# Optimization experiments

Measured on AMD Instinct MI355X. Metric: run time of the kernel, lower is better.

The kernel has to match this reference:

```python
import jax, jax.numpy as jnp
import numpy as np

B, T, C = 4, 2048, 1024
H, D = 16, 64  # n_heads, head_dim; C == H*D

def setup_inputs() -> dict:
    key = jax.random.key(0)
    ks = jax.random.split(key, 6)
    s_in = 1.0 / np.sqrt(C)
    x = jax.random.normal(ks[0], (B, T, C), dtype=jnp.float32)
    # causal mask: True above the diagonal -> masked to -inf
    mask = jnp.triu(jnp.ones((T, T), dtype=bool), k=1)
    Wqkv = jax.random.uniform(ks[1], (C, 3 * C), jnp.float32, -s_in, s_in)
    bqkv = jax.random.uniform(ks[2], (3 * C,), jnp.float32, -s_in, s_in)
    Wout = jax.random.uniform(ks[3], (C, C), jnp.float32, -s_in, s_in)
    bout = jax.random.uniform(ks[4], (C,), jnp.float32, -s_in, s_in)
    return {"x": x, "mask": mask, "Wqkv": Wqkv, "bqkv": bqkv, "Wout": Wout, "bout": bout}

def reference(x, mask, Wqkv, bqkv, Wout, bout):
    b, t, c = x.shape
    qkv = (x @ Wqkv + bqkv).reshape(b, t, 3, H, D)
    qkv = jnp.transpose(qkv, (2, 0, 3, 1, 4))  # [3, B, H, T, D]
    q, k, v = qkv[0], qkv[1], qkv[2]
    scores = jnp.einsum("bhqd,bhkd->bhqk", q, k) / jnp.sqrt(jnp.float32(D))
    scores = jnp.where(mask[:t, :t][None, None, :, :], -jnp.inf, scores)
    attn = jax.nn.softmax(scores, axis=-1)
    out = jnp.einsum("bhqk,bhkd->bhqd", attn, v)
    out = jnp.transpose(out, (0, 2, 1, 3)).reshape(b, t, c)
    return out @ Wout + bout
```

## Files before the change

### kernel.cpp

```cpp
#include <hip/hip_runtime.h>

typedef unsigned short u16;
typedef __attribute__((ext_vector_type(8))) short bf16x8;
typedef __attribute__((ext_vector_type(4))) short bf16x4;
typedef __attribute__((ext_vector_type(4))) float f32x4;

#define MFMA16(a, b, c) __builtin_amdgcn_mfma_f32_16x16x32_bf16(a, b, c, 0, 0, 0)

__device__ __forceinline__ u16 f2bf(float x) {
    unsigned u = __float_as_uint(x);
    return (u16)((u + 0x7fffu + ((u >> 16) & 1u)) >> 16);
}
__device__ __forceinline__ u16 f2bf_fast(float x) {
    return (u16)((__float_as_uint(x) + 0x8000u) >> 16);
}

__global__ __launch_bounds__(256) void castk(const float* __restrict__ src, u16* __restrict__ dst) {
    const int i = (blockIdx.x * 256 + threadIdx.x) * 8;
    float4 a = *(const float4*)(src + i);
    float4 b = *(const float4*)(src + i + 4);
    bf16x8 v;
    v[0] = (short)f2bf(a.x); v[1] = (short)f2bf(a.y);
    v[2] = (short)f2bf(a.z); v[3] = (short)f2bf(a.w);
    v[4] = (short)f2bf(b.x); v[5] = (short)f2bf(b.y);
    v[6] = (short)f2bf(b.z); v[7] = (short)f2bf(b.w);
    *(bf16x8*)(dst + i) = v;
}

__global__ __launch_bounds__(256) void tkern(const float* __restrict__ src, u16* __restrict__ dst,
                                             int R, int C) {
    const int tC = C >> 6;
    const int tr = (blockIdx.x / tC) << 6;
    const int tc = (blockIdx.x % tC) << 6;
    __shared__ u16 ls[64 * 68];
    const int tid = threadIdx.x;
#pragma unroll
    for (int rep = 0; rep < 2; ++rep) {
        const int f = tid * 8 + rep * 2048;
        const int r = f >> 6, c = f & 63;
        float4 a = *(const float4*)(src + (size_t)(tr + r) * C + tc + c);
        float4 b = *(const float4*)(src + (size_t)(tr + r) * C + tc + c + 4);
        bf16x4 lo, hi;
        lo[0] = (short)f2bf(a.x); lo[1] = (short)f2bf(a.y);
        lo[2] = (short)f2bf(a.z); lo[3] = (short)f2bf(a.w);
        hi[0] = (short)f2bf(b.x); hi[1] = (short)f2bf(b.y);
        hi[2] = (short)f2bf(b.z); hi[3] = (short)f2bf(b.w);
        *(bf16x4*)&ls[r * 68 + c] = lo;
        *(bf16x4*)&ls[r * 68 + c + 4] = hi;
    }
    __syncthreads();
#pragma unroll
    for (int rep = 0; rep < 2; ++rep) {
        const int f = tid * 8 + rep * 2048;
        const int rn = f >> 6, ck = f & 63;
        bf16x8 v;
#pragma unroll
        for (int j = 0; j < 8; ++j) v[j] = (short)ls[(ck + j) * 68 + rn];
        *(bf16x8*)(dst + (size_t)(tc + rn) * R + tr + ck) = v;
    }
}

template <int MODE>
__global__ __launch_bounds__(256) void gemm_k(const u16* __restrict__ A, const u16* __restrict__ Bt,
                                              const float* __restrict__ bias,
                                              u16* __restrict__ Qo, u16* __restrict__ Ko,
                                              u16* __restrict__ Vo, float* __restrict__ Of) {
    constexpr int Kd = 1024;
    const int tid = threadIdx.x;
    const int lane = tid & 63, wave = tid >> 6;
    const int wm = wave >> 1, wn = wave & 1;
    const int lr = lane & 15, lg = lane >> 4;
    const int mt = blockIdx.x & 63;
    const int nt = blockIdx.x >> 6;
    const int mbase = mt << 7, nbase = nt << 7;
    __shared__ u16 As[128 * 32];
    __shared__ u16 Bs[128 * 32];
    f32x4 acc[4][4];
#pragma unroll
    for (int i = 0; i < 4; ++i)
#pragma unroll
        for (int j = 0; j < 4; ++j) acc[i][j] = {0.f, 0.f, 0.f, 0.f};

    for (int kb = 0; kb < Kd; kb += 32) {
        __syncthreads();
#pragma unroll
        for (int rep = 0; rep < 2; ++rep) {
            const int f = tid * 8 + rep * 2048;
            const int r = f >> 5, c = f & 31;
            __builtin_amdgcn_global_load_lds(
                (const __attribute__((address_space(1))) void*)(A + (size_t)(mbase + r) * Kd + kb + c),
                (__attribute__((address_space(3))) void*)(As + f), 16, 0, 0);
            __builtin_amdgcn_global_load_lds(
                (const __attribute__((address_space(1))) void*)(Bt + (size_t)(nbase + r) * Kd + kb + c),
                (__attribute__((address_space(3))) void*)(Bs + f), 16, 0, 0);
        }
        __syncthreads();
        bf16x8 af[4], bfr[4];
#pragma unroll
        for (int i = 0; i < 4; ++i)
            af[i] = *(const bf16x8*)&As[(wm * 64 + i * 16 + lr) * 32 + lg * 8];
#pragma unroll
        for (int j = 0; j < 4; ++j)
            bfr[j] = *(const bf16x8*)&Bs[(wn * 64 + j * 16 + lr) * 32 + lg * 8];
#pragma unroll
        for (int i = 0; i < 4; ++i)
#pragma unroll
            for (int j = 0; j < 4; ++j) acc[i][j] = MFMA16(af[i], bfr[j], acc[i][j]);
    }

    const float QSCALE = 0.1803368801111137f;
#pragma unroll
    for (int j = 0; j < 4; ++j) {
        const int n = nbase + wn * 64 + j * 16 + lr;
        const float bj = bias[n];
        if (MODE == 0) {
            const int three = n >> 10;
            const int h = (n >> 6) & 15;
            const int d = n & 63;
#pragma unroll
            for (int i = 0; i < 4; ++i) {
#pragma unroll
                for (int r = 0; r < 4; ++r) {
                    const int m = mbase + wm * 64 + i * 16 + lg * 4 + r;
                    const int b = m >> 11, t = m & 2047;
                    const int bh = (b << 4) + h;
                    const float val = acc[i][j][r] + bj;
                    if (three == 0)
                        Qo[(((size_t)bh << 11) + t) * 64 + d] = f2bf(val * QSCALE);
                    else if (three == 1)
                        Ko[(((size_t)bh << 11) + t) * 64 + d] = f2bf(val);
                    else
                        Vo[(((size_t)bh << 6) + d) * 2048 + t] = f2bf(val);
                }
            }
        } else {
#pragma unroll
            for (int i = 0; i < 4; ++i) {
#pragma unroll
                for (int r = 0; r < 4; ++r) {
                    const int m = mbase + wm * 64 + i * 16 + lg * 4 + r;
                    Of[((size_t)m << 10) + n] = acc[i][j][r] + bj;
                }
            }
        }
    }
}

__global__ __launch_bounds__(128, 2) void flash_attn(const u16* __restrict__ Q, const u16* __restrict__ Kg,
                                                     const u16* __restrict__ Vt, u16* __restrict__ Aout) {
    const int tid = threadIdx.x;
    const int lane = tid & 63, wave = tid >> 6;
    const int lr = lane & 15, lg = lane >> 4;
    const int bx = blockIdx.x;
    const int bh = blockIdx.y;
    const int b = bh >> 4, h = bh & 15;
    const size_t base = (size_t)bh << 17;

    const int qb_hi = 16 + bx;
    const int qb_lo = 15 - bx;

    __shared__ u16 Ps[2][16 * 72];

    int qbase[4];
    qbase[0] = qb_hi * 64 + wave * 32;
    qbase[1] = qbase[0] + 16;
    qbase[2] = qb_lo * 64 + wave * 32;
    qbase[3] = qbase[2] + 16;

    bf16x8 qf[4][2];
#pragma unroll
    for (int st = 0; st < 4; ++st) {
        const u16* p = Q + base + (size_t)(qbase[st] + lr) * 64;
        qf[st][0] = *(const bf16x8*)(p + lg * 8);
        qf[st][1] = *(const bf16x8*)(p + 32 + lg * 8);
    }

    f32x4 o[4][4];
#pragma unroll
    for (int st = 0; st < 4; ++st)
#pragma unroll
        for (int dt = 0; dt < 4; ++dt) o[st][dt] = {0.f, 0.f, 0.f, 0.f};
    float m_[4] = {-INFINITY, -INFINITY, -INFINITY, -INFINITY};
    float l_[4] = {0.f, 0.f, 0.f, 0.f};

    const u16* Kbase = Kg + base + (size_t)lr * 64 + lg * 8;
    const u16* Vbase = Vt + base + (size_t)lr * 2048 + lg * 8;

    for (int kt = 0; kt <= qb_hi; ++kt) {
        bf16x8 kf[4][2], vf[4][2];
        const u16* kp = Kbase + (size_t)kt * 4096;
#pragma unroll
        for (int rt = 0; rt < 4; ++rt) {
            kf[rt][0] = *(const bf16x8*)(kp + rt * 1024);
            kf[rt][1] = *(const bf16x8*)(kp + rt * 1024 + 32);
        }
        const u16* vp = Vbase + kt * 64;
#pragma unroll
        for (int dt = 0; dt < 4; ++dt) {
            vf[dt][0] = *(const bf16x8*)(vp + dt * 32768);
            vf[dt][1] = *(const bf16x8*)(vp + dt * 32768 + 32);
        }

        auto process = [&](int st, bool diag) {
            f32x4 s[4];
#pragma unroll
            for (int rt = 0; rt < 4; ++rt) {
                f32x4 z = {0.f, 0.f, 0.f, 0.f};
                z = MFMA16(kf[rt][0], qf[st][0], z);
                z = MFMA16(kf[rt][1], qf[st][1], z);
                s[rt] = z;
            }
            if (diag) {
                const int q_glob = qbase[st] + lr;
#pragma unroll
                for (int rt = 0; rt < 4; ++rt)
#pragma unroll
                    for (int r = 0; r < 4; ++r) {
                        const int kv = kt * 64 + rt * 16 + lg * 4 + r;
                        if (kv > q_glob) s[rt][r] = -INFINITY;
                    }
            }
            float rmax = -INFINITY;
#pragma unroll
            for (int rt = 0; rt < 4; ++rt)
#pragma unroll
                for (int r = 0; r < 4; ++r) rmax = fmaxf(rmax, s[rt][r]);
            rmax = fmaxf(rmax, __shfl_xor(rmax, 16));
            rmax = fmaxf(rmax, __shfl_xor(rmax, 32));
            const float m_new = fmaxf(m_[st], rmax);
            const float alpha = exp2f(m_[st] - m_new);
            float rsum = 0.f;
#pragma unroll
            for (int rt = 0; rt < 4; ++rt)
#pragma unroll
                for (int r = 0; r < 4; ++r) {
                    const float p = exp2f(s[rt][r] - m_new);
                    s[rt][r] = p;
                    rsum += p;
                }
            rsum += __shfl_xor(rsum, 16);
            rsum += __shfl_xor(rsum, 32);
            l_[st] = l_[st] * alpha + rsum;
            m_[st] = m_new;

#pragma unroll
            for (int rt = 0; rt < 4; ++rt) {
                bf16x4 pk;
#pragma unroll
                for (int r = 0; r < 4; ++r) pk[r] = (short)f2bf_fast(s[rt][r]);
                *(bf16x4*)&Ps[wave][lr * 72 + rt * 16 + lg * 4] = pk;
            }
            float aq[4];
#pragma unroll
            for (int r = 0; r < 4; ++r) aq[r] = __shfl(alpha, (lane & 48) + lg * 4 + r);
#pragma unroll
            for (int dt = 0; dt < 4; ++dt)
#pragma unroll
                for (int r = 0; r < 4; ++r) o[st][dt][r] *= aq[r];

            const bf16x8 pf0 = *(const bf16x8*)&Ps[wave][lr * 72 + lg * 8];
            const bf16x8 pf1 = *(const bf16x8*)&Ps[wave][lr * 72 + 32 + lg * 8];
#pragma unroll
            for (int dt = 0; dt < 4; ++dt) {
                o[st][dt] = MFMA16(pf0, vf[dt][0], o[st][dt]);
                o[st][dt] = MFMA16(pf1, vf[dt][1], o[st][dt]);
            }
        };

        process(0, kt == qb_hi);
        process(1, kt == qb_hi);
        if (kt <= qb_lo) {
            process(2, kt == qb_lo);
            process(3, kt == qb_lo);
        }
    }

#pragma unroll
    for (int st = 0; st < 4; ++st) {
        const float linv = 1.f / l_[st];
        float lq[4];
#pragma unroll
        for (int r = 0; r < 4; ++r) lq[r] = __shfl(linv, (lane & 48) + lg * 4 + r);
#pragma unroll
        for (int dt = 0; dt < 4; ++dt)
#pragma unroll
            for (int r = 0; r < 4; ++r) {
                const int t = qbase[st] + lg * 4 + r;
                Aout[(((size_t)(b << 11) + t) << 10) + h * 64 + dt * 16 + lr] =
                    f2bf(o[st][dt][r] * lq[r]);
            }
    }
}

extern "C" void kernel_launch(void* const* d_in, const int* in_sizes, int n_in,
                              void* d_out, int out_size, void* d_ws, size_t ws_size,
                              hipStream_t stream) {
    (void)in_sizes; (void)n_in; (void)out_size; (void)ws_size;
    const float* x    = (const float*)d_in[0];
    const float* Wqkv = (const float*)d_in[2];
    const float* bqkv = (const float*)d_in[3];
    const float* Wout = (const float*)d_in[4];
    const float* bout = (const float*)d_in[5];
    float* out = (float*)d_out;

    char* ws = (char*)d_ws;
    u16* WqkvT = (u16*)(ws);
    u16* WoutT = (u16*)(ws + 6291456);
    u16* xb    = (u16*)(ws + 8388608);
    u16* Qb    = (u16*)(ws + 25165824);
    u16* Kb    = (u16*)(ws + 41943040);
    u16* Vtb   = (u16*)(ws + 58720256);
    u16* Ab    = (u16*)(ws + 75497472);

    castk<<<dim3(4096), 256, 0, stream>>>(x, xb);
    tkern<<<dim3(16 * 48), 256, 0, stream>>>(Wqkv, WqkvT, 1024, 3072);
    tkern<<<dim3(16 * 16), 256, 0, stream>>>(Wout, WoutT, 1024, 1024);
    gemm_k<0><<<dim3(64 * 24), 256, 0, stream>>>(xb, WqkvT, bqkv, Qb, Kb, Vtb, nullptr);
    flash_attn<<<dim3(16, 64), 128, 0, stream>>>(Qb, Kb, Vtb, Ab);
    gemm_k<1><<<dim3(64 * 8), 256, 0, stream>>>(Ab, WoutT, bout, nullptr, nullptr, nullptr, out);
}
```

Before: 336.9 us.

## Double-buffer K loads and transpose PV MFMA to drop alpha shuffles

Prefetches the next K tile into a second register buffer while the current tile is processed. It swaps the MFMA operand order for P·V so each lane holds output rows matching its own softmax statistics. That removes the alpha and 1/l shuffles and allows vectorized 4-wide bf16 stores of the output. The rescale of O is also skipped when no row's max changed, at the cost of higher register pressure from the double buffer.

```diff
diff --git a/kernel.cpp b/kernel.cpp
--- a/kernel.cpp
+++ b/kernel.cpp
@@ -186,14 +186,21 @@
     const u16* Kbase = Kg + base + (size_t)lr * 64 + lg * 8;
     const u16* Vbase = Vt + base + (size_t)lr * 2048 + lg * 8;
 
-    for (int kt = 0; kt <= qb_hi; ++kt) {
-        bf16x8 kf[4][2], vf[4][2];
+    auto loadK = [&](int kt, bf16x8 (&kf)[4][2]) {
         const u16* kp = Kbase + (size_t)kt * 4096;
 #pragma unroll
         for (int rt = 0; rt < 4; ++rt) {
             kf[rt][0] = *(const bf16x8*)(kp + rt * 1024);
             kf[rt][1] = *(const bf16x8*)(kp + rt * 1024 + 32);
         }
+    };
+
+    bf16x8 kfA[4][2], kfB[4][2];
+    loadK(0, kfA);
+
+    auto iter = [&](int kt, bf16x8 (&kf)[4][2], bf16x8 (&kfN)[4][2]) {
+        loadK(kt < qb_hi ? kt + 1 : qb_hi, kfN);
+        bf16x8 vf[4][2];
         const u16* vp = Vbase + kt * 64;
 #pragma unroll
         for (int dt = 0; dt < 4; ++dt) {
@@ -250,20 +257,18 @@
                 for (int r = 0; r < 4; ++r) pk[r] = (short)f2bf_fast(s[rt][r]);
                 *(bf16x4*)&Ps[wave][lr * 72 + rt * 16 + lg * 4] = pk;
             }
-            float aq[4];
-#pragma unroll
-            for (int r = 0; r < 4; ++r) aq[r] = __shfl(alpha, (lane & 48) + lg * 4 + r);
-#pragma unroll
-            for (int dt = 0; dt < 4; ++dt)
-#pragma unroll
-                for (int r = 0; r < 4; ++r) o[st][dt][r] *= aq[r];
-
+            if (__any(alpha != 1.0f)) {
+#pragma unroll
+                for (int dt = 0; dt < 4; ++dt)
+#pragma unroll
+                    for (int r = 0; r < 4; ++r) o[st][dt][r] *= alpha;
+            }
             const bf16x8 pf0 = *(const bf16x8*)&Ps[wave][lr * 72 + lg * 8];
             const bf16x8 pf1 = *(const bf16x8*)&Ps[wave][lr * 72 + 32 + lg * 8];
 #pragma unroll
             for (int dt = 0; dt < 4; ++dt) {
-                o[st][dt] = MFMA16(pf0, vf[dt][0], o[st][dt]);
-                o[st][dt] = MFMA16(pf1, vf[dt][1], o[st][dt]);
+                o[st][dt] = MFMA16(vf[dt][0], pf0, o[st][dt]);
+                o[st][dt] = MFMA16(vf[dt][1], pf1, o[st][dt]);
             }
         };
 
@@ -273,22 +278,27 @@
             process(2, kt == qb_lo);
             process(3, kt == qb_lo);
         }
+    };
+
+    for (int kt = 0; kt <= qb_hi;) {
+        iter(kt, kfA, kfB);
+        ++kt;
+        if (kt > qb_hi) break;
+        iter(kt, kfB, kfA);
+        ++kt;
     }
 
 #pragma unroll
     for (int st = 0; st < 4; ++st) {
         const float linv = 1.f / l_[st];
-        float lq[4];
-#pragma unroll
-        for (int r = 0; r < 4; ++r) lq[r] = __shfl(linv, (lane & 48) + lg * 4 + r);
-#pragma unroll
-        for (int dt = 0; dt < 4; ++dt)
-#pragma unroll
-            for (int r = 0; r < 4; ++r) {
-                const int t = qbase[st] + lg * 4 + r;
-                Aout[(((size_t)(b << 11) + t) << 10) + h * 64 + dt * 16 + lr] =
-                    f2bf(o[st][dt][r] * lq[r]);
-            }
+        const int t = qbase[st] + lr;
+#pragma unroll
+        for (int dt = 0; dt < 4; ++dt) {
+            bf16x4 pk;
+#pragma unroll
+            for (int r = 0; r < 4; ++r) pk[r] = (short)f2bf(o[st][dt][r] * linv);
+            *(bf16x4*)&Aout[(((size_t)(b << 11) + t) << 10) + h * 64 + dt * 16 + lg * 4] = pk;
+        }
     }
 }
 
```

Measured after the change: 413.8 us. 1.23x slower.

## Split flash attention across four waves and transpose PV output layout

Applied to the files above, without the earlier changes.

The attention block now uses 256 threads with four waves, each owning 16 query rows of the high and low query tiles, instead of two waves with 32 rows each. This cuts per-wave register state and allows higher occupancy. The P·V MFMA operands are swapped so the output accumulators are indexed by query along the lane. That makes the row-wise rescale factor and 1/l available per lane without shuffles, and allows vectorized bf16x4 stores. The rescale of the accumulators is skipped when no lane's running max changed. In exchange, each wave now loads the K and V tiles separately, so more waves read the same K/V per block, raising cache and global traffic.

```diff
diff --git a/kernel.cpp b/kernel.cpp
--- a/kernel.cpp
+++ b/kernel.cpp
@@ -146,7 +146,51 @@
     }
 }
 
-__global__ __launch_bounds__(128, 2) void flash_attn(const u16* __restrict__ Q, const u16* __restrict__ Kg,
+__device__ __forceinline__ float fa_softmax_pack(f32x4 (&s)[4], float& m_i, float& l_i,
+                                                 int ktbase, int q_glob, bool diag,
+                                                 int lr, int lg, u16* __restrict__ Psw) {
+    if (diag) {
+#pragma unroll
+        for (int rt = 0; rt < 4; ++rt)
+#pragma unroll
+            for (int r = 0; r < 4; ++r) {
+                const int kv = ktbase + rt * 16 + lg * 4 + r;
+                if (kv > q_glob) s[rt][r] = -INFINITY;
+            }
+    }
+    float rmax = -INFINITY;
+#pragma unroll
+    for (int rt = 0; rt < 4; ++rt)
+#pragma unroll
+        for (int r = 0; r < 4; ++r) rmax = fmaxf(rmax, s[rt][r]);
+    rmax = fmaxf(rmax, __shfl_xor(rmax, 16));
+    rmax = fmaxf(rmax, __shfl_xor(rmax, 32));
+    const float m_new = fmaxf(m_i, rmax);
+    const float alpha = exp2f(m_i - m_new);
+    float rsum = 0.f;
+#pragma unroll
+    for (int rt = 0; rt < 4; ++rt)
+#pragma unroll
+        for (int r = 0; r < 4; ++r) {
+            const float p = exp2f(s[rt][r] - m_new);
+            s[rt][r] = p;
+            rsum += p;
+        }
+    rsum += __shfl_xor(rsum, 16);
+    rsum += __shfl_xor(rsum, 32);
+    l_i = l_i * alpha + rsum;
+    m_i = m_new;
+#pragma unroll
+    for (int rt = 0; rt < 4; ++rt) {
+        bf16x4 pk;
+#pragma unroll
+        for (int r = 0; r < 4; ++r) pk[r] = (short)f2bf_fast(s[rt][r]);
+        *(bf16x4*)&Psw[lr * 72 + rt * 16 + lg * 4] = pk;
+    }
+    return alpha;
+}
+
+__global__ __launch_bounds__(256, 4) void flash_attn(const u16* __restrict__ Q, const u16* __restrict__ Kg,
                                                      const u16* __restrict__ Vt, u16* __restrict__ Aout) {
     const int tid = threadIdx.x;
     const int lane = tid & 63, wave = tid >> 6;
@@ -159,136 +203,112 @@
     const int qb_hi = 16 + bx;
     const int qb_lo = 15 - bx;
 
-    __shared__ u16 Ps[2][16 * 72];
-
-    int qbase[4];
-    qbase[0] = qb_hi * 64 + wave * 32;
-    qbase[1] = qbase[0] + 16;
-    qbase[2] = qb_lo * 64 + wave * 32;
-    qbase[3] = qbase[2] + 16;
-
-    bf16x8 qf[4][2];
-#pragma unroll
-    for (int st = 0; st < 4; ++st) {
-        const u16* p = Q + base + (size_t)(qbase[st] + lr) * 64;
-        qf[st][0] = *(const bf16x8*)(p + lg * 8);
-        qf[st][1] = *(const bf16x8*)(p + 32 + lg * 8);
-    }
-
-    f32x4 o[4][4];
-#pragma unroll
-    for (int st = 0; st < 4; ++st)
-#pragma unroll
-        for (int dt = 0; dt < 4; ++dt) o[st][dt] = {0.f, 0.f, 0.f, 0.f};
-    float m_[4] = {-INFINITY, -INFINITY, -INFINITY, -INFINITY};
-    float l_[4] = {0.f, 0.f, 0.f, 0.f};
+    __shared__ u16 Ps[4][2][16 * 72];
+
+    const int qbase_h = qb_hi * 64 + wave * 16;
+    const int qbase_l = qb_lo * 64 + wave * 16;
+
+    bf16x8 qfh0, qfh1, qfl0, qfl1;
+    {
+        const u16* p = Q + base + (size_t)(qbase_h + lr) * 64;
+        qfh0 = *(const bf16x8*)(p + lg * 8);
+        qfh1 = *(const bf16x8*)(p + 32 + lg * 8);
+        const u16* q = Q + base + (size_t)(qbase_l + lr) * 64;
+        qfl0 = *(const bf16x8*)(q + lg * 8);
+        qfl1 = *(const bf16x8*)(q + 32 + lg * 8);
+    }
+
+    f32x4 oh[4], ol[4];
+#pragma unroll
+    for (int dt = 0; dt < 4; ++dt) { oh[dt] = {0.f, 0.f, 0.f, 0.f}; ol[dt] = {0.f, 0.f, 0.f, 0.f}; }
+    float mh = -INFINITY, lh = 0.f, ml = -INFINITY, ll = 0.f;
 
     const u16* Kbase = Kg + base + (size_t)lr * 64 + lg * 8;
     const u16* Vbase = Vt + base + (size_t)lr * 2048 + lg * 8;
 
     for (int kt = 0; kt <= qb_hi; ++kt) {
-        bf16x8 kf[4][2], vf[4][2];
+        const bool lo_act = (kt <= qb_lo);
+
+        f32x4 sh[4], sl[4];
         const u16* kp = Kbase + (size_t)kt * 4096;
 #pragma unroll
         for (int rt = 0; rt < 4; ++rt) {
-            kf[rt][0] = *(const bf16x8*)(kp + rt * 1024);
-            kf[rt][1] = *(const bf16x8*)(kp + rt * 1024 + 32);
+            const bf16x8 k0 = *(const bf16x8*)(kp + rt * 1024);
+            const bf16x8 k1 = *(const bf16x8*)(kp + rt * 1024 + 32);
+            f32x4 z = {0.f, 0.f, 0.f, 0.f};
+            z = MFMA16(k0, qfh0, z);
+            z = MFMA16(k1, qfh1, z);
+            sh[rt] = z;
+            if (lo_act) {
+                f32x4 y = {0.f, 0.f, 0.f, 0.f};
+                y = MFMA16(k0, qfl0, y);
+                y = MFMA16(k1, qfl1, y);
+                sl[rt] = y;
+            }
+        }
+
+        const float ah = fa_softmax_pack(sh, mh, lh, kt * 64, qbase_h + lr, kt == qb_hi,
+                                         lr, lg, Ps[wave][0]);
+        float al = 1.f;
+        if (lo_act)
+            al = fa_softmax_pack(sl, ml, ll, kt * 64, qbase_l + lr, kt == qb_lo,
+                                 lr, lg, Ps[wave][1]);
+
+        if (__any(ah != 1.0f)) {
+#pragma unroll
+            for (int dt = 0; dt < 4; ++dt)
+#pragma unroll
+                for (int r = 0; r < 4; ++r) oh[dt][r] *= ah;
+        }
+        if (lo_act && __any(al != 1.0f)) {
+#pragma unroll
+            for (int dt = 0; dt < 4; ++dt)
+#pragma unroll
+                for (int r = 0; r < 4; ++r) ol[dt][r] *= al;
+        }
+
+        const bf16x8 pfh0 = *(const bf16x8*)&Ps[wave][0][lr * 72 + lg * 8];
+        const bf16x8 pfh1 = *(const bf16x8*)&Ps[wave][0][lr * 72 + 32 + lg * 8];
+        bf16x8 pfl0, pfl1;
+        if (lo_act) {
+            pfl0 = *(const bf16x8*)&Ps[wave][1][lr * 72 + lg * 8];
+            pfl1 = *(const bf16x8*)&Ps[wave][1][lr * 72 + 32 + lg * 8];
         }
         const u16* vp = Vbase + kt * 64;
 #pragma unroll
         for (int dt = 0; dt < 4; ++dt) {
-            vf[dt][0] = *(const bf16x8*)(vp + dt * 32768);
-            vf[dt][1] = *(const bf16x8*)(vp + dt * 32768 + 32);
-        }
-
-        auto process = [&](int st, bool diag) {
-            f32x4 s[4];
-#pragma unroll
-            for (int rt = 0; rt < 4; ++rt) {
-                f32x4 z = {0.f, 0.f, 0.f, 0.f};
-                z = MFMA16(kf[rt][0], qf[st][0], z);
-                z = MFMA16(kf[rt][1], qf[st][1], z);
-                s[rt] = z;
-            }
-            if (diag) {
-                const int q_glob = qbase[st] + lr;
-#pragma unroll
-                for (int rt = 0; rt < 4; ++rt)
-#pragma unroll
-                    for (int r = 0; r < 4; ++r) {
-                        const int kv = kt * 64 + rt * 16 + lg * 4 + r;
-                        if (kv > q_glob) s[rt][r] = -INFINITY;
-                    }
-            }
-            float rmax = -INFINITY;
-#pragma unroll
-            for (int rt = 0; rt < 4; ++rt)
-#pragma unroll
-                for (int r = 0; r < 4; ++r) rmax = fmaxf(rmax, s[rt][r]);
-            rmax = fmaxf(rmax, __shfl_xor(rmax, 16));
-            rmax = fmaxf(rmax, __shfl_xor(rmax, 32));
-            const float m_new = fmaxf(m_[st], rmax);
-            const float alpha = exp2f(m_[st] - m_new);
-            float rsum = 0.f;
-#pragma unroll
-            for (int rt = 0; rt < 4; ++rt)
-#pragma unroll
-                for (int r = 0; r < 4; ++r) {
-                    const float p = exp2f(s[rt][r] - m_new);
-                    s[rt][r] = p;
-                    rsum += p;
-                }
-            rsum += __shfl_xor(rsum, 16);
-            rsum += __shfl_xor(rsum, 32);
-            l_[st] = l_[st] * alpha + rsum;
-            m_[st] = m_new;
-
-#pragma unroll
-            for (int rt = 0; rt < 4; ++rt) {
-                bf16x4 pk;
-#pragma unroll
-                for (int r = 0; r < 4; ++r) pk[r] = (short)f2bf_fast(s[rt][r]);
-                *(bf16x4*)&Ps[wave][lr * 72 + rt * 16 + lg * 4] = pk;
-            }
-            float aq[4];
-#pragma unroll
-            for (int r = 0; r < 4; ++r) aq[r] = __shfl(alpha, (lane & 48) + lg * 4 + r);
-#pragma unroll
-            for (int dt = 0; dt < 4; ++dt)
-#pragma unroll
-                for (int r = 0; r < 4; ++r) o[st][dt][r] *= aq[r];
-
-            const bf16x8 pf0 = *(const bf16x8*)&Ps[wave][lr * 72 + lg * 8];
-            const bf16x8 pf1 = *(const bf16x8*)&Ps[wave][lr * 72 + 32 + lg * 8];
-#pragma unroll
-            for (int dt = 0; dt < 4; ++dt) {
-                o[st][dt] = MFMA16(pf0, vf[dt][0], o[st][dt]);
-                o[st][dt] = MFMA16(pf1, vf[dt][1], o[st][dt]);
-            }
-        };
-
-        process(0, kt == qb_hi);
-        process(1, kt == qb_hi);
-        if (kt <= qb_lo) {
-            process(2, kt == qb_lo);
-            process(3, kt == qb_lo);
-        }
-    }
-
-#pragma unroll
-    for (int st = 0; st < 4; ++st) {
-        const float linv = 1.f / l_[st];
-        float lq[4];
-#pragma unroll
-        for (int r = 0; r < 4; ++r) lq[r] = __shfl(linv, (lane & 48) + lg * 4 + r);
-#pragma unroll
-        for (int dt = 0; dt < 4; ++dt)
-#pragma unroll
-            for (int r = 0; r < 4; ++r) {
-                const int t = qbase[st] + lg * 4 + r;
-                Aout[(((size_t)(b << 11) + t) << 10) + h * 64 + dt * 16 + lr] =
-                    f2bf(o[st][dt][r] * lq[r]);
-            }
+            const bf16x8 v0 = *(const bf16x8*)(vp + dt * 32768);
+            const bf16x8 v1 = *(const bf16x8*)(vp + dt * 32768 + 32);
+            oh[dt] = MFMA16(v0, pfh0, oh[dt]);
+            oh[dt] = MFMA16(v1, pfh1, oh[dt]);
+            if (lo_act) {
+                ol[dt] = MFMA16(v0, pfl0, ol[dt]);
+                ol[dt] = MFMA16(v1, pfl1, ol[dt]);
+            }
+        }
+    }
+
+    {
+        const float linv = 1.f / lh;
+        const int t = qbase_h + lr;
+#pragma unroll
+        for (int dt = 0; dt < 4; ++dt) {
+            bf16x4 pk;
+#pragma unroll
+            for (int r = 0; r < 4; ++r) pk[r] = (short)f2bf(oh[dt][r] * linv);
+            *(bf16x4*)&Aout[(((size_t)(b << 11) + t) << 10) + h * 64 + dt * 16 + lg * 4] = pk;
+        }
+    }
+    {
+        const float linv = 1.f / ll;
+        const int t = qbase_l + lr;
+#pragma unroll
+        for (int dt = 0; dt < 4; ++dt) {
+            bf16x4 pk;
+#pragma unroll
+            for (int r = 0; r < 4; ++r) pk[r] = (short)f2bf(ol[dt][r] * linv);
+            *(bf16x4*)&Aout[(((size_t)(b << 11) + t) << 10) + h * 64 + dt * 16 + lg * 4] = pk;
+        }
     }
 }
 
@@ -316,6 +336,6 @@
     tkern<<<dim3(16 * 48), 256, 0, stream>>>(Wqkv, WqkvT, 1024, 3072);
     tkern<<<dim3(16 * 16), 256, 0, stream>>>(Wout, WoutT, 1024, 1024);
     gemm_k<0><<<dim3(64 * 24), 256, 0, stream>>>(xb, WqkvT, bqkv, Qb, Kb, Vtb, nullptr);
-    flash_attn<<<dim3(16, 64), 128, 0, stream>>>(Qb, Kb, Vtb, Ab);
+    flash_attn<<<dim3(16, 64), 256, 0, stream>>>(Qb, Kb, Vtb, Ab);
     gemm_k<1><<<dim3(64 * 8), 256, 0, stream>>>(Ab, WoutT, bout, nullptr, nullptr, nullptr, out);
 }
```

After: 445.5 us. 1.32x slower.
